# Performance work log

Measured on AMD Instinct MI355X. Metric: run time of the kernel, lower is better.

## Reference

```python
import jax, jax.numpy as jnp
import numpy as np

B = 65536
LAYERS = [256, 512, 512, 256]


def setup_inputs() -> dict:
    key = jax.random.key(0)
    ks = jax.random.split(key, 10)
    inp = {"data": jax.random.normal(ks[0], (B, LAYERS[0]), dtype=jnp.float32)}
    for i in range(3):
        n_in, n_out = LAYERS[i], LAYERS[i + 1]
        # link weights ~ U[0,1) like random.random(); bias params[0] zeroed in torch code
        inp[f"W{i+1}"] = jax.random.uniform(ks[1 + 3 * i], (n_in, n_out), dtype=jnp.float32)
        inp[f"b{i+1}"] = jnp.zeros((n_out,), dtype=jnp.float32)
        # per-node activation params a = params[1:6], torch.rand init
        inp[f"a{i+1}"] = jax.random.uniform(ks[2 + 3 * i], (n_out, 5), dtype=jnp.float32)
    return inp


def _act(x, a):
    # x: [B, n], a: [n, 5]; a0*tanh(x)*sin(a1*x+a2) + a3*x + a4  (per-node params broadcast over batch)
    return a[:, 0] * jnp.tanh(x) * jnp.sin(a[:, 1] * x + a[:, 2]) + a[:, 3] * x + a[:, 4]


def reference(data, W1, b1, a1, W2, b2, a2, W3, b3, a3):
    h = _act(data @ W1 + b1, a1)
    h = _act(h @ W2 + b2, a2)
    h = _act(h @ W3 + b3, a3)
    return jax.nn.softmax(h, axis=1)
```

## Files before the change

### kernel.cpp

```cpp
#include <hip/hip_runtime.h>

#define BATCH 65536

typedef float f32x4 __attribute__((ext_vector_type(4)));
typedef _Float16 f16x8 __attribute__((ext_vector_type(8)));

__device__ __forceinline__ void async_ld16(const void* g, void* l) {
  __builtin_amdgcn_global_load_lds(
      (const __attribute__((address_space(1))) void*)g,
      (__attribute__((address_space(3))) void*)l, 16, 0, 0);
}

__device__ __forceinline__ float act_f(float x, float a0, float a1, float a2,
                                       float a3, float a4) {
  float ax = fabsf(x);
  float e = __builtin_amdgcn_exp2f(ax * -2.8853900817779268f);
  float th = (1.0f - e) * __builtin_amdgcn_rcpf(1.0f + e);
  th = copysignf(th, x);
  float arg = fmaf(a1, x, a2);
  float rev = arg * 0.15915494309189535f;
  rev -= floorf(rev);
  float s = __builtin_amdgcn_sinf(rev);
  return fmaf(a3, x, fmaf(a0 * th, s, a4));
}

__global__ __launch_bounds__(256) void splitT_k(const float* __restrict__ W,
                                                _Float16* __restrict__ hi,
                                                _Float16* __restrict__ lo,
                                                int K, int N) {
  const int i = blockIdx.x * 256 + threadIdx.x;
  if (i >= K * N) return;
  const int k = i / N, n = i % N;
  const float w = W[i];
  const _Float16 h = (_Float16)w;
  hi[(size_t)n * K + k] = h;
  lo[(size_t)n * K + k] = (_Float16)(w - (float)h);
}

template <bool AF32, bool FINAL>
__global__ __launch_bounds__(256, 2) void gemm_act(
    const float* __restrict__ Af, const _Float16* __restrict__ Ahi,
    const _Float16* __restrict__ Alo, const _Float16* __restrict__ Bhi,
    const _Float16* __restrict__ Blo, const float* __restrict__ bias,
    const float* __restrict__ ap, _Float16* __restrict__ Chi,
    _Float16* __restrict__ Clo, float* __restrict__ Cout, int K, int N) {
  __shared__ __align__(16) _Float16 sA[AF32 ? 2 : 2 * 128 * 32];
  __shared__ __align__(16) _Float16 sB[2 * 128 * 32];

  const int tid = threadIdx.x;
  const int wv = tid >> 6;
  const int lane = tid & 63;
  const int wm = wv >> 1, wn = wv & 1;
  const int m16 = lane & 15, quad = lane >> 4;
  const int col0 = blockIdx.x * 128;
  const int row0 = blockIdx.y * 128;
  const int crow = lane >> 2;
  const int cseg = lane & 3;

  f32x4 acc[4][4];
  const f32x4 zero = {0.f, 0.f, 0.f, 0.f};
#pragma unroll
  for (int i = 0; i < 4; ++i)
#pragma unroll
    for (int j = 0; j < 4; ++j) acc[i][j] = zero;

  const int nk = K >> 5;
  for (int kt = 0; kt < nk; ++kt) {
    const int k0 = kt << 5;
    if (!AF32) {
#pragma unroll
      for (int t = 0; t < 2; ++t) {
        const int c = wv * 2 + t;
        const int r = c * 16 + crow;
        const size_t ga = (size_t)(row0 + r) * K + k0 + cseg * 8;
        async_ld16(Ahi + ga, (void*)&sA[c * 512]);
        async_ld16(Alo + ga, (void*)&sA[128 * 32 + c * 512]);
      }
    }
#pragma unroll
    for (int t = 0; t < 2; ++t) {
      const int c = wv * 2 + t;
      const int r = c * 16 + crow;
      const size_t gb = (size_t)(col0 + r) * K + k0 + cseg * 8;
      async_ld16(Bhi + gb, (void*)&sB[c * 512]);
      async_ld16(Blo + gb, (void*)&sB[128 * 32 + c * 512]);
    }

    f16x8 ah[4], al[4], bh[4], bl[4];
    if (AF32) {
#pragma unroll
      for (int tm = 0; tm < 4; ++tm) {
        const float* p =
            Af + (size_t)(row0 + wm * 64 + tm * 16 + m16) * K + k0 + quad * 8;
        const f32x4 x0 = *(const f32x4*)p;
        const f32x4 x1 = *(const f32x4*)(p + 4);
#pragma unroll
        for (int j = 0; j < 4; ++j) {
          const _Float16 h0 = (_Float16)x0[j];
          ah[tm][j] = h0;
          al[tm][j] = (_Float16)(x0[j] - (float)h0);
          const _Float16 h1 = (_Float16)x1[j];
          ah[tm][4 + j] = h1;
          al[tm][4 + j] = (_Float16)(x1[j] - (float)h1);
        }
      }
    }
    __syncthreads();

    if (!AF32) {
#pragma unroll
      for (int tm = 0; tm < 4; ++tm) {
        const int idx = (wm * 64 + tm * 16 + m16) * 32 + quad * 8;
        ah[tm] = *(const f16x8*)&sA[idx];
        al[tm] = *(const f16x8*)&sA[128 * 32 + idx];
      }
    }
#pragma unroll
    for (int tn = 0; tn < 4; ++tn) {
      const int idx = (wn * 64 + tn * 16 + m16) * 32 + quad * 8;
      bh[tn] = *(const f16x8*)&sB[idx];
      bl[tn] = *(const f16x8*)&sB[128 * 32 + idx];
    }
#pragma unroll
    for (int tm = 0; tm < 4; ++tm)
#pragma unroll
      for (int tn = 0; tn < 4; ++tn) {
        acc[tm][tn] = __builtin_amdgcn_mfma_f32_16x16x32_f16(ah[tm], bh[tn],
                                                             acc[tm][tn], 0, 0, 0);
        acc[tm][tn] = __builtin_amdgcn_mfma_f32_16x16x32_f16(ah[tm], bl[tn],
                                                             acc[tm][tn], 0, 0, 0);
        acc[tm][tn] = __builtin_amdgcn_mfma_f32_16x16x32_f16(al[tm], bh[tn],
                                                             acc[tm][tn], 0, 0, 0);
      }
    __syncthreads();
  }

#pragma unroll
  for (int tn = 0; tn < 4; ++tn) {
    const int col = col0 + wn * 64 + tn * 16 + m16;
    const float bs = bias[col];
    const float p0 = ap[col * 5 + 0];
    const float p1 = ap[col * 5 + 1];
    const float p2 = ap[col * 5 + 2];
    const float p3 = ap[col * 5 + 3];
    const float p4 = ap[col * 5 + 4];
#pragma unroll
    for (int tm = 0; tm < 4; ++tm) {
      const int row = row0 + wm * 64 + tm * 16 + quad * 4;
#pragma unroll
      for (int r = 0; r < 4; ++r) {
        const float y = act_f(acc[tm][tn][r] + bs, p0, p1, p2, p3, p4);
        const size_t o = (size_t)(row + r) * N + col;
        if (FINAL) {
          Cout[o] = y;
        } else {
          const _Float16 h = (_Float16)y;
          Chi[o] = h;
          Clo[o] = (_Float16)(y - (float)h);
        }
      }
    }
  }
}

__global__ __launch_bounds__(256) void softmax_rows(float* __restrict__ io) {
  const int wv = threadIdx.x >> 6, lane = threadIdx.x & 63;
  const size_t row = (size_t)blockIdx.x * 4 + wv;
  f32x4* p = (f32x4*)(io + row * 256);
  f32x4 v = p[lane];
  float m = fmaxf(fmaxf(v[0], v[1]), fmaxf(v[2], v[3]));
#pragma unroll
  for (int off = 32; off > 0; off >>= 1) m = fmaxf(m, __shfl_xor(m, off));
  f32x4 e;
  float s = 0.f;
#pragma unroll
  for (int j = 0; j < 4; ++j) {
    e[j] = __builtin_amdgcn_exp2f((v[j] - m) * 1.4426950408889634f);
    s += e[j];
  }
#pragma unroll
  for (int off = 32; off > 0; off >>= 1) s += __shfl_xor(s, off);
  const float inv = __builtin_amdgcn_rcpf(s);
#pragma unroll
  for (int j = 0; j < 4; ++j) e[j] *= inv;
  p[lane] = e;
}

extern "C" void kernel_launch(void* const* d_in, const int* in_sizes, int n_in,
                              void* d_out, int out_size, void* d_ws,
                              size_t ws_size, hipStream_t stream) {
  const float* data = (const float*)d_in[0];
  const float* W1 = (const float*)d_in[1];
  const float* b1 = (const float*)d_in[2];
  const float* a1 = (const float*)d_in[3];
  const float* W2 = (const float*)d_in[4];
  const float* b2 = (const float*)d_in[5];
  const float* a2 = (const float*)d_in[6];
  const float* W3 = (const float*)d_in[7];
  const float* b3 = (const float*)d_in[8];
  const float* a3 = (const float*)d_in[9];
  float* out = (float*)d_out;

  char* ws = (char*)d_ws;
  const size_t KB = 1024, MB = 1024 * 1024;
  _Float16* w1hi = (_Float16*)(ws + 0 * KB);
  _Float16* w1lo = (_Float16*)(ws + 256 * KB);
  _Float16* w2hi = (_Float16*)(ws + 512 * KB);
  _Float16* w2lo = (_Float16*)(ws + 1024 * KB);
  _Float16* w3hi = (_Float16*)(ws + 1536 * KB);
  _Float16* w3lo = (_Float16*)(ws + 1792 * KB);
  char* hb = ws + 2 * MB;

  const size_t avail = (ws_size > 2 * MB) ? ws_size - 2 * MB : 0;
  int R = BATCH;
  while ((size_t)R * 4096 > avail && R > 1024) R >>= 1;
  _Float16* h1hi = (_Float16*)(hb);
  _Float16* h1lo = (_Float16*)(hb + (size_t)R * 1024);
  _Float16* h2hi = (_Float16*)(hb + (size_t)R * 2048);
  _Float16* h2lo = (_Float16*)(hb + (size_t)R * 3072);

  splitT_k<<<(256 * 512 + 255) / 256, 256, 0, stream>>>(W1, w1hi, w1lo, 256, 512);
  splitT_k<<<(512 * 512 + 255) / 256, 256, 0, stream>>>(W2, w2hi, w2lo, 512, 512);
  splitT_k<<<(512 * 256 + 255) / 256, 256, 0, stream>>>(W3, w3hi, w3lo, 512, 256);

  for (int c0 = 0; c0 < BATCH; c0 += R) {
    const float* dc = data + (size_t)c0 * 256;
    float* oc = out + (size_t)c0 * 256;
    gemm_act<true, false><<<dim3(512 / 128, R / 128), 256, 0, stream>>>(
        dc, nullptr, nullptr, w1hi, w1lo, b1, a1, h1hi, h1lo, nullptr, 256, 512);
    gemm_act<false, false><<<dim3(512 / 128, R / 128), 256, 0, stream>>>(
        nullptr, h1hi, h1lo, w2hi, w2lo, b2, a2, h2hi, h2lo, nullptr, 512, 512);
    gemm_act<false, true><<<dim3(256 / 128, R / 128), 256, 0, stream>>>(
        nullptr, h2hi, h2lo, w3hi, w3lo, b3, a3, nullptr, nullptr, oc, 512, 256);
  }

  softmax_rows<<<BATCH / 4, 256, 0, stream>>>(out);
}
```

Measured before the change: 515.1 us.

## Fuse all three MLP layers and softmax into one kernel with LDS-resident activations

Replaces the three per-layer GEMM launches and the separate softmax kernel with a single kernel. Each block handles 32 batch rows and keeps the intermediate activations (split into hi/lo fp16) in a 64KB XOR-swizzled shared buffer, then applies softmax before writing out. This removes the global-memory round trips of the intermediate h1/h2 tensors and the logits. In exchange, weights are streamed directly from global/L2 into registers per block without LDS staging, so every block rereads the full weight matrices. The small row tile also reduces per-block reuse of those weights.

```diff
diff --git a/kernel.cpp b/kernel.cpp
--- a/kernel.cpp
+++ b/kernel.cpp
@@ -4,12 +4,6 @@
 
 typedef float f32x4 __attribute__((ext_vector_type(4)));
 typedef _Float16 f16x8 __attribute__((ext_vector_type(8)));
-
-__device__ __forceinline__ void async_ld16(const void* g, void* l) {
-  __builtin_amdgcn_global_load_lds(
-      (const __attribute__((address_space(1))) void*)g,
-      (__attribute__((address_space(3))) void*)l, 16, 0, 0);
-}
 
 __device__ __forceinline__ float act_f(float x, float a0, float a1, float a2,
                                        float a3, float a4) {
@@ -37,107 +31,53 @@
   lo[(size_t)n * K + k] = (_Float16)(w - (float)h);
 }
 
-template <bool AF32, bool FINAL>
-__global__ __launch_bounds__(256, 2) void gemm_act(
-    const float* __restrict__ Af, const _Float16* __restrict__ Ahi,
-    const _Float16* __restrict__ Alo, const _Float16* __restrict__ Bhi,
-    const _Float16* __restrict__ Blo, const float* __restrict__ bias,
-    const float* __restrict__ ap, _Float16* __restrict__ Chi,
-    _Float16* __restrict__ Clo, float* __restrict__ Cout, int K, int N) {
-  __shared__ __align__(16) _Float16 sA[AF32 ? 2 : 2 * 128 * 32];
-  __shared__ __align__(16) _Float16 sB[2 * 128 * 32];
-
-  const int tid = threadIdx.x;
-  const int wv = tid >> 6;
-  const int lane = tid & 63;
-  const int wm = wv >> 1, wn = wv & 1;
-  const int m16 = lane & 15, quad = lane >> 4;
-  const int col0 = blockIdx.x * 128;
-  const int row0 = blockIdx.y * 128;
-  const int crow = lane >> 2;
-  const int cseg = lane & 3;
-
-  f32x4 acc[4][4];
-  const f32x4 zero = {0.f, 0.f, 0.f, 0.f};
-#pragma unroll
-  for (int i = 0; i < 4; ++i)
-#pragma unroll
-    for (int j = 0; j < 4; ++j) acc[i][j] = zero;
-
-  const int nk = K >> 5;
-  for (int kt = 0; kt < nk; ++kt) {
-    const int k0 = kt << 5;
-    if (!AF32) {
-#pragma unroll
-      for (int t = 0; t < 2; ++t) {
-        const int c = wv * 2 + t;
-        const int r = c * 16 + crow;
-        const size_t ga = (size_t)(row0 + r) * K + k0 + cseg * 8;
-        async_ld16(Ahi + ga, (void*)&sA[c * 512]);
-        async_ld16(Alo + ga, (void*)&sA[128 * 32 + c * 512]);
-      }
-    }
-#pragma unroll
-    for (int t = 0; t < 2; ++t) {
-      const int c = wv * 2 + t;
-      const int r = c * 16 + crow;
-      const size_t gb = (size_t)(col0 + r) * K + k0 + cseg * 8;
-      async_ld16(Bhi + gb, (void*)&sB[c * 512]);
-      async_ld16(Blo + gb, (void*)&sB[128 * 32 + c * 512]);
-    }
-
-    f16x8 ah[4], al[4], bh[4], bl[4];
-    if (AF32) {
-#pragma unroll
-      for (int tm = 0; tm < 4; ++tm) {
-        const float* p =
-            Af + (size_t)(row0 + wm * 64 + tm * 16 + m16) * K + k0 + quad * 8;
-        const f32x4 x0 = *(const f32x4*)p;
-        const f32x4 x1 = *(const f32x4*)(p + 4);
-#pragma unroll
-        for (int j = 0; j < 4; ++j) {
-          const _Float16 h0 = (_Float16)x0[j];
-          ah[tm][j] = h0;
-          al[tm][j] = (_Float16)(x0[j] - (float)h0);
-          const _Float16 h1 = (_Float16)x1[j];
-          ah[tm][4 + j] = h1;
-          al[tm][4 + j] = (_Float16)(x1[j] - (float)h1);
-        }
-      }
-    }
-    __syncthreads();
-
-    if (!AF32) {
-#pragma unroll
-      for (int tm = 0; tm < 4; ++tm) {
-        const int idx = (wm * 64 + tm * 16 + m16) * 32 + quad * 8;
-        ah[tm] = *(const f16x8*)&sA[idx];
-        al[tm] = *(const f16x8*)&sA[128 * 32 + idx];
-      }
-    }
-#pragma unroll
-    for (int tn = 0; tn < 4; ++tn) {
-      const int idx = (wn * 64 + tn * 16 + m16) * 32 + quad * 8;
-      bh[tn] = *(const f16x8*)&sB[idx];
-      bl[tn] = *(const f16x8*)&sB[128 * 32 + idx];
-    }
-#pragma unroll
-    for (int tm = 0; tm < 4; ++tm)
-#pragma unroll
-      for (int tn = 0; tn < 4; ++tn) {
-        acc[tm][tn] = __builtin_amdgcn_mfma_f32_16x16x32_f16(ah[tm], bh[tn],
-                                                             acc[tm][tn], 0, 0, 0);
-        acc[tm][tn] = __builtin_amdgcn_mfma_f32_16x16x32_f16(ah[tm], bl[tn],
-                                                             acc[tm][tn], 0, 0, 0);
-        acc[tm][tn] = __builtin_amdgcn_mfma_f32_16x16x32_f16(al[tm], bh[tn],
-                                                             acc[tm][tn], 0, 0, 0);
-      }
-    __syncthreads();
-  }
-
-#pragma unroll
-  for (int tn = 0; tn < 4; ++tn) {
-    const int col = col0 + wn * 64 + tn * 16 + m16;
+__device__ __forceinline__ f32x4 mfma3(f16x8 ah, f16x8 al, f16x8 bh, f16x8 bl,
+                                       f32x4 c) {
+  c = __builtin_amdgcn_mfma_f32_16x16x32_f16(ah, bh, c, 0, 0, 0);
+  c = __builtin_amdgcn_mfma_f32_16x16x32_f16(ah, bl, c, 0, 0, 0);
+  c = __builtin_amdgcn_mfma_f32_16x16x32_f16(al, bh, c, 0, 0, 0);
+  return c;
+}
+
+template <int NT, int NK>
+__device__ __forceinline__ void layer_h(const _Float16* __restrict__ hb,
+                                        const _Float16* __restrict__ Bhi,
+                                        const _Float16* __restrict__ Blo,
+                                        int K, int wv, int m16, int quad,
+                                        f32x4 acc[2][8]) {
+#pragma unroll 2
+  for (int it = 0; it < NK; ++it) {
+    f16x8 bh[NT], bl[NT];
+    const int nbase = (wv * NT * 16 + m16) * K + it * 32 + quad * 8;
+#pragma unroll
+    for (int tn = 0; tn < NT; ++tn) {
+      bh[tn] = *(const f16x8*)(Bhi + nbase + tn * 16 * K);
+      bl[tn] = *(const f16x8*)(Blo + nbase + tn * 16 * K);
+    }
+    f16x8 ah[2], al[2];
+    const int ks = (it * 32 + quad * 8) ^ (m16 << 3);
+#pragma unroll
+    for (int tm = 0; tm < 2; ++tm) {
+      const int ro = (tm * 16 + m16) * 1024;
+      ah[tm] = *(const f16x8*)&hb[ro + ks];
+      al[tm] = *(const f16x8*)&hb[ro + 512 + ks];
+    }
+#pragma unroll
+    for (int tn = 0; tn < NT; ++tn)
+#pragma unroll
+      for (int tm = 0; tm < 2; ++tm)
+        acc[tm][tn] = mfma3(ah[tm], al[tm], bh[tn], bl[tn], acc[tm][tn]);
+  }
+}
+
+template <int NT, bool TO_H>
+__device__ __forceinline__ void epilogue(f32x4 acc[2][8],
+                                         const float* __restrict__ bias,
+                                         const float* __restrict__ ap, int wv,
+                                         int m16, int quad, _Float16* hb) {
+#pragma unroll
+  for (int tn = 0; tn < NT; ++tn) {
+    const int col = wv * NT * 16 + tn * 16 + m16;
     const float bs = bias[col];
     const float p0 = ap[col * 5 + 0];
     const float p1 = ap[col * 5 + 1];
@@ -145,45 +85,136 @@
     const float p3 = ap[col * 5 + 3];
     const float p4 = ap[col * 5 + 4];
 #pragma unroll
-    for (int tm = 0; tm < 4; ++tm) {
-      const int row = row0 + wm * 64 + tm * 16 + quad * 4;
+    for (int tm = 0; tm < 2; ++tm)
 #pragma unroll
       for (int r = 0; r < 4; ++r) {
+        const int row = tm * 16 + quad * 4 + r;
         const float y = act_f(acc[tm][tn][r] + bs, p0, p1, p2, p3, p4);
-        const size_t o = (size_t)(row + r) * N + col;
-        if (FINAL) {
-          Cout[o] = y;
+        if (TO_H) {
+          const int cs = col ^ ((row & 15) << 3);
+          const _Float16 h = (_Float16)y;
+          hb[row * 1024 + cs] = h;
+          hb[row * 1024 + 512 + cs] = (_Float16)(y - (float)h);
         } else {
-          const _Float16 h = (_Float16)y;
-          Chi[o] = h;
-          Clo[o] = (_Float16)(y - (float)h);
+          ((float*)hb)[row * 256 + col] = y;
         }
       }
-    }
-  }
-}
-
-__global__ __launch_bounds__(256) void softmax_rows(float* __restrict__ io) {
-  const int wv = threadIdx.x >> 6, lane = threadIdx.x & 63;
-  const size_t row = (size_t)blockIdx.x * 4 + wv;
-  f32x4* p = (f32x4*)(io + row * 256);
-  f32x4 v = p[lane];
-  float m = fmaxf(fmaxf(v[0], v[1]), fmaxf(v[2], v[3]));
-#pragma unroll
-  for (int off = 32; off > 0; off >>= 1) m = fmaxf(m, __shfl_xor(m, off));
-  f32x4 e;
-  float s = 0.f;
-#pragma unroll
-  for (int j = 0; j < 4; ++j) {
-    e[j] = __builtin_amdgcn_exp2f((v[j] - m) * 1.4426950408889634f);
-    s += e[j];
-  }
-#pragma unroll
-  for (int off = 32; off > 0; off >>= 1) s += __shfl_xor(s, off);
-  const float inv = __builtin_amdgcn_rcpf(s);
-#pragma unroll
-  for (int j = 0; j < 4; ++j) e[j] *= inv;
-  p[lane] = e;
+  }
+}
+
+__global__ __launch_bounds__(256, 2) void fused_net(
+    const float* __restrict__ data, const _Float16* __restrict__ w1hi,
+    const _Float16* __restrict__ w1lo, const float* __restrict__ b1,
+    const float* __restrict__ a1p, const _Float16* __restrict__ w2hi,
+    const _Float16* __restrict__ w2lo, const float* __restrict__ b2,
+    const float* __restrict__ a2p, const _Float16* __restrict__ w3hi,
+    const _Float16* __restrict__ w3lo, const float* __restrict__ b3,
+    const float* __restrict__ a3p, float* __restrict__ out) {
+  __shared__ __align__(16) _Float16 hb[32 * 1024];
+
+  const int tid = threadIdx.x;
+  const int wv = tid >> 6, lane = tid & 63;
+  const int m16 = lane & 15, quad = lane >> 4;
+  const int row0 = blockIdx.x * 32;
+
+  float* dptr = (float*)hb;
+
+  {
+    const float* dg = data + (size_t)row0 * 256;
+#pragma unroll
+    for (int i = 0; i < 8; ++i) {
+      const int idx = tid + i * 256;
+      const int r = idx >> 6, c4 = (idx & 63) << 2;
+      const f32x4 v = *(const f32x4*)(dg + r * 256 + c4);
+      const int cs = c4 ^ ((r & 15) << 3);
+      *(f32x4*)&dptr[r * 256 + cs] = v;
+    }
+  }
+  __syncthreads();
+
+  f32x4 acc[2][8];
+  const f32x4 zero = {0.f, 0.f, 0.f, 0.f};
+
+#pragma unroll
+  for (int i = 0; i < 2; ++i)
+#pragma unroll
+    for (int j = 0; j < 8; ++j) acc[i][j] = zero;
+#pragma unroll 2
+  for (int it = 0; it < 8; ++it) {
+    f16x8 bh[8], bl[8];
+    const int nbase = (wv * 128 + m16) * 256 + it * 32 + quad * 8;
+#pragma unroll
+    for (int tn = 0; tn < 8; ++tn) {
+      bh[tn] = *(const f16x8*)(w1hi + nbase + tn * 16 * 256);
+      bl[tn] = *(const f16x8*)(w1lo + nbase + tn * 16 * 256);
+    }
+    f16x8 ah[2], al[2];
+    const int ks = (it * 32 + quad * 8) ^ (m16 << 3);
+#pragma unroll
+    for (int tm = 0; tm < 2; ++tm) {
+      const int ro = (tm * 16 + m16) * 256;
+      const f32x4 x0 = *(const f32x4*)&dptr[ro + ks];
+      const f32x4 x1 = *(const f32x4*)&dptr[ro + ks + 4];
+#pragma unroll
+      for (int j = 0; j < 4; ++j) {
+        const _Float16 h0 = (_Float16)x0[j];
+        ah[tm][j] = h0;
+        al[tm][j] = (_Float16)(x0[j] - (float)h0);
+        const _Float16 h1 = (_Float16)x1[j];
+        ah[tm][4 + j] = h1;
+        al[tm][4 + j] = (_Float16)(x1[j] - (float)h1);
+      }
+    }
+#pragma unroll
+    for (int tn = 0; tn < 8; ++tn)
+#pragma unroll
+      for (int tm = 0; tm < 2; ++tm)
+        acc[tm][tn] = mfma3(ah[tm], al[tm], bh[tn], bl[tn], acc[tm][tn]);
+  }
+  __syncthreads();
+  epilogue<8, true>(acc, b1, a1p, wv, m16, quad, hb);
+  __syncthreads();
+
+#pragma unroll
+  for (int i = 0; i < 2; ++i)
+#pragma unroll
+    for (int j = 0; j < 8; ++j) acc[i][j] = zero;
+  layer_h<8, 16>(hb, w2hi, w2lo, 512, wv, m16, quad, acc);
+  __syncthreads();
+  epilogue<8, true>(acc, b2, a2p, wv, m16, quad, hb);
+  __syncthreads();
+
+#pragma unroll
+  for (int i = 0; i < 2; ++i)
+#pragma unroll
+    for (int j = 0; j < 8; ++j) acc[i][j] = zero;
+  layer_h<4, 16>(hb, w3hi, w3lo, 512, wv, m16, quad, acc);
+  __syncthreads();
+  epilogue<4, false>(acc, b3, a3p, wv, m16, quad, hb);
+  __syncthreads();
+
+  const float* lg = (const float*)hb;
+#pragma unroll
+  for (int r8 = 0; r8 < 8; ++r8) {
+    const int row = wv * 8 + r8;
+    f32x4 v = *(const f32x4*)&lg[row * 256 + lane * 4];
+    float m = fmaxf(fmaxf(v[0], v[1]), fmaxf(v[2], v[3]));
+#pragma unroll
+    for (int off = 32; off > 0; off >>= 1) m = fmaxf(m, __shfl_xor(m, off));
+    f32x4 e;
+    float s = 0.f;
+#pragma unroll
+    for (int j = 0; j < 4; ++j) {
+      e[j] = __builtin_amdgcn_exp2f((v[j] - m) * 1.4426950408889634f);
+      s += e[j];
+    }
+#pragma unroll
+    for (int off = 32; off > 0; off >>= 1) s += __shfl_xor(s, off);
+    const float inv = __builtin_amdgcn_rcpf(s);
+#pragma unroll
+    for (int j = 0; j < 4; ++j) e[j] *= inv;
+    *(f32x4*)(out + (size_t)(row0 + row) * 256 + lane * 4) = e;
+  }
 }
 
 extern "C" void kernel_launch(void* const* d_in, const int* in_sizes, int n_in,
@@ -202,37 +233,19 @@
   float* out = (float*)d_out;
 
   char* ws = (char*)d_ws;
-  const size_t KB = 1024, MB = 1024 * 1024;
+  const size_t KB = 1024;
   _Float16* w1hi = (_Float16*)(ws + 0 * KB);
   _Float16* w1lo = (_Float16*)(ws + 256 * KB);
   _Float16* w2hi = (_Float16*)(ws + 512 * KB);
   _Float16* w2lo = (_Float16*)(ws + 1024 * KB);
   _Float16* w3hi = (_Float16*)(ws + 1536 * KB);
   _Float16* w3lo = (_Float16*)(ws + 1792 * KB);
-  char* hb = ws + 2 * MB;
-
-  const size_t avail = (ws_size > 2 * MB) ? ws_size - 2 * MB : 0;
-  int R = BATCH;
-  while ((size_t)R * 4096 > avail && R > 1024) R >>= 1;
-  _Float16* h1hi = (_Float16*)(hb);
-  _Float16* h1lo = (_Float16*)(hb + (size_t)R * 1024);
-  _Float16* h2hi = (_Float16*)(hb + (size_t)R * 2048);
-  _Float16* h2lo = (_Float16*)(hb + (size_t)R * 3072);
 
   splitT_k<<<(256 * 512 + 255) / 256, 256, 0, stream>>>(W1, w1hi, w1lo, 256, 512);
   splitT_k<<<(512 * 512 + 255) / 256, 256, 0, stream>>>(W2, w2hi, w2lo, 512, 512);
   splitT_k<<<(512 * 256 + 255) / 256, 256, 0, stream>>>(W3, w3hi, w3lo, 512, 256);
 
-  for (int c0 = 0; c0 < BATCH; c0 += R) {
-    const float* dc = data + (size_t)c0 * 256;
-    float* oc = out + (size_t)c0 * 256;
-    gemm_act<true, false><<<dim3(512 / 128, R / 128), 256, 0, stream>>>(
-        dc, nullptr, nullptr, w1hi, w1lo, b1, a1, h1hi, h1lo, nullptr, 256, 512);
-    gemm_act<false, false><<<dim3(512 / 128, R / 128), 256, 0, stream>>>(
-        nullptr, h1hi, h1lo, w2hi, w2lo, b2, a2, h2hi, h2lo, nullptr, 512, 512);
-    gemm_act<false, true><<<dim3(256 / 128, R / 128), 256, 0, stream>>>(
-        nullptr, h2hi, h2lo, w3hi, w3lo, b3, a3, nullptr, nullptr, oc, 512, 256);
-  }
-
-  softmax_rows<<<BATCH / 4, 256, 0, stream>>>(out);
-}
+  fused_net<<<BATCH / 32, 256, 0, stream>>>(data, w1hi, w1lo, b1, a1, w2hi,
+                                            w2lo, b2, a2, w3hi, w3lo, b3, a3,
+                                            out);
+}
```

Result: slower. 605.2 us (+17.5%).

## Retile fused GEMM+activation to 64x256 blocks and stage fp32 input through LDS

Applied to the files above, without the earlier changes.

Changes the block tile from 128x128 to 64 rows by 256 columns, so each block covers all or half of the output columns. B fragments are reused across two M sub-tiles, and the launch bound asks for 4 blocks per CU instead of 2. The first layer now copies fp32 input into LDS with async loads instead of reading it directly from global per wave. The batch chunking loop is dropped and the layer-2 hi buffer is placed in the output buffer, which assumes a large enough workspace. This adds LDS use and register pressure, with fewer blocks along N.

```diff
diff --git a/kernel.cpp b/kernel.cpp
--- a/kernel.cpp
+++ b/kernel.cpp
@@ -37,63 +37,75 @@
   lo[(size_t)n * K + k] = (_Float16)(w - (float)h);
 }
 
+__device__ __forceinline__ f32x4 mfma3(f16x8 ah, f16x8 al, f16x8 bh, f16x8 bl,
+                                       f32x4 c) {
+  c = __builtin_amdgcn_mfma_f32_16x16x32_f16(ah, bh, c, 0, 0, 0);
+  c = __builtin_amdgcn_mfma_f32_16x16x32_f16(ah, bl, c, 0, 0, 0);
+  c = __builtin_amdgcn_mfma_f32_16x16x32_f16(al, bh, c, 0, 0, 0);
+  return c;
+}
+
 template <bool AF32, bool FINAL>
-__global__ __launch_bounds__(256, 2) void gemm_act(
+__global__ __launch_bounds__(256, 4) void gemm_act(
     const float* __restrict__ Af, const _Float16* __restrict__ Ahi,
     const _Float16* __restrict__ Alo, const _Float16* __restrict__ Bhi,
     const _Float16* __restrict__ Blo, const float* __restrict__ bias,
     const float* __restrict__ ap, _Float16* __restrict__ Chi,
     _Float16* __restrict__ Clo, float* __restrict__ Cout, int K, int N) {
-  __shared__ __align__(16) _Float16 sA[AF32 ? 2 : 2 * 128 * 32];
-  __shared__ __align__(16) _Float16 sB[2 * 128 * 32];
+  __shared__ __align__(16) _Float16 sA[4096];
+  __shared__ __align__(16) _Float16 sB[16384];
 
   const int tid = threadIdx.x;
   const int wv = tid >> 6;
   const int lane = tid & 63;
   const int wm = wv >> 1, wn = wv & 1;
   const int m16 = lane & 15, quad = lane >> 4;
-  const int col0 = blockIdx.x * 128;
-  const int row0 = blockIdx.y * 128;
-  const int crow = lane >> 2;
-  const int cseg = lane & 3;
-
-  f32x4 acc[4][4];
+  const int col0 = blockIdx.x * 256;
+  const int row0 = blockIdx.y * 64;
+
+  f32x4 acc[2][8];
   const f32x4 zero = {0.f, 0.f, 0.f, 0.f};
 #pragma unroll
-  for (int i = 0; i < 4; ++i)
-#pragma unroll
-    for (int j = 0; j < 4; ++j) acc[i][j] = zero;
+  for (int i = 0; i < 2; ++i)
+#pragma unroll
+    for (int j = 0; j < 8; ++j) acc[i][j] = zero;
 
   const int nk = K >> 5;
   for (int kt = 0; kt < nk; ++kt) {
     const int k0 = kt << 5;
-    if (!AF32) {
+    if (AF32) {
+      float* sAf = (float*)sA;
 #pragma unroll
       for (int t = 0; t < 2; ++t) {
         const int c = wv * 2 + t;
-        const int r = c * 16 + crow;
-        const size_t ga = (size_t)(row0 + r) * K + k0 + cseg * 8;
-        async_ld16(Ahi + ga, (void*)&sA[c * 512]);
-        async_ld16(Alo + ga, (void*)&sA[128 * 32 + c * 512]);
+        const int r = c * 8 + (lane >> 3);
+        const size_t ga = (size_t)(row0 + r) * K + k0 + (lane & 7) * 4;
+        async_ld16(Af + ga, (void*)&sAf[c * 256]);
       }
-    }
-#pragma unroll
-    for (int t = 0; t < 2; ++t) {
-      const int c = wv * 2 + t;
-      const int r = c * 16 + crow;
-      const size_t gb = (size_t)(col0 + r) * K + k0 + cseg * 8;
+    } else {
+      const int r = wv * 16 + (lane >> 2);
+      const size_t ga = (size_t)(row0 + r) * K + k0 + (lane & 3) * 8;
+      async_ld16(Ahi + ga, (void*)&sA[wv * 512]);
+      async_ld16(Alo + ga, (void*)&sA[2048 + wv * 512]);
+    }
+#pragma unroll
+    for (int t = 0; t < 4; ++t) {
+      const int c = wv * 4 + t;
+      const int col = c * 16 + (lane >> 2);
+      const size_t gb = (size_t)(col0 + col) * K + k0 + (lane & 3) * 8;
       async_ld16(Bhi + gb, (void*)&sB[c * 512]);
-      async_ld16(Blo + gb, (void*)&sB[128 * 32 + c * 512]);
-    }
-
-    f16x8 ah[4], al[4], bh[4], bl[4];
-    if (AF32) {
-#pragma unroll
-      for (int tm = 0; tm < 4; ++tm) {
-        const float* p =
-            Af + (size_t)(row0 + wm * 64 + tm * 16 + m16) * K + k0 + quad * 8;
-        const f32x4 x0 = *(const f32x4*)p;
-        const f32x4 x1 = *(const f32x4*)(p + 4);
+      async_ld16(Blo + gb, (void*)&sB[8192 + c * 512]);
+    }
+    __syncthreads();
+
+    f16x8 ah[2], al[2];
+#pragma unroll
+    for (int tm = 0; tm < 2; ++tm) {
+      const int arow = wm * 32 + tm * 16 + m16;
+      if (AF32) {
+        const float* pa = (const float*)sA + arow * 32 + quad * 8;
+        const f32x4 x0 = *(const f32x4*)pa;
+        const f32x4 x1 = *(const f32x4*)(pa + 4);
 #pragma unroll
         for (int j = 0; j < 4; ++j) {
           const _Float16 h0 = (_Float16)x0[j];
@@ -103,41 +115,26 @@
           ah[tm][4 + j] = h1;
           al[tm][4 + j] = (_Float16)(x1[j] - (float)h1);
         }
+      } else {
+        ah[tm] = *(const f16x8*)&sA[arow * 32 + quad * 8];
+        al[tm] = *(const f16x8*)&sA[2048 + arow * 32 + quad * 8];
       }
     }
-    __syncthreads();
-
-    if (!AF32) {
-#pragma unroll
-      for (int tm = 0; tm < 4; ++tm) {
-        const int idx = (wm * 64 + tm * 16 + m16) * 32 + quad * 8;
-        ah[tm] = *(const f16x8*)&sA[idx];
-        al[tm] = *(const f16x8*)&sA[128 * 32 + idx];
-      }
-    }
-#pragma unroll
-    for (int tn = 0; tn < 4; ++tn) {
-      const int idx = (wn * 64 + tn * 16 + m16) * 32 + quad * 8;
-      bh[tn] = *(const f16x8*)&sB[idx];
-      bl[tn] = *(const f16x8*)&sB[128 * 32 + idx];
-    }
-#pragma unroll
-    for (int tm = 0; tm < 4; ++tm)
-#pragma unroll
-      for (int tn = 0; tn < 4; ++tn) {
-        acc[tm][tn] = __builtin_amdgcn_mfma_f32_16x16x32_f16(ah[tm], bh[tn],
-                                                             acc[tm][tn], 0, 0, 0);
-        acc[tm][tn] = __builtin_amdgcn_mfma_f32_16x16x32_f16(ah[tm], bl[tn],
-                                                             acc[tm][tn], 0, 0, 0);
-        acc[tm][tn] = __builtin_amdgcn_mfma_f32_16x16x32_f16(al[tm], bh[tn],
-                                                             acc[tm][tn], 0, 0, 0);
-      }
+#pragma unroll
+    for (int tn = 0; tn < 8; ++tn) {
+      const int bcol = wn * 128 + tn * 16 + m16;
+      const f16x8 bh = *(const f16x8*)&sB[bcol * 32 + quad * 8];
+      const f16x8 bl = *(const f16x8*)&sB[8192 + bcol * 32 + quad * 8];
+#pragma unroll
+      for (int tm = 0; tm < 2; ++tm)
+        acc[tm][tn] = mfma3(ah[tm], al[tm], bh, bl, acc[tm][tn]);
+    }
     __syncthreads();
   }
 
 #pragma unroll
-  for (int tn = 0; tn < 4; ++tn) {
-    const int col = col0 + wn * 64 + tn * 16 + m16;
+  for (int tn = 0; tn < 8; ++tn) {
+    const int col = col0 + wn * 128 + tn * 16 + m16;
     const float bs = bias[col];
     const float p0 = ap[col * 5 + 0];
     const float p1 = ap[col * 5 + 1];
@@ -145,15 +142,15 @@
     const float p3 = ap[col * 5 + 3];
     const float p4 = ap[col * 5 + 4];
 #pragma unroll
-    for (int tm = 0; tm < 4; ++tm) {
-      const int row = row0 + wm * 64 + tm * 16 + quad * 4;
+    for (int tm = 0; tm < 2; ++tm) {
+      const int row = row0 + wm * 32 + tm * 16 + quad * 4;
 #pragma unroll
       for (int r = 0; r < 4; ++r) {
         const float y = act_f(acc[tm][tn][r] + bs, p0, p1, p2, p3, p4);
-        const size_t o = (size_t)(row + r) * N + col;
         if (FINAL) {
-          Cout[o] = y;
+          Cout[(size_t)(row + r) * 256 + col] = y;
         } else {
+          const size_t o = (size_t)(row + r) * N + col;
           const _Float16 h = (_Float16)y;
           Chi[o] = h;
           Clo[o] = (_Float16)(y - (float)h);
@@ -209,30 +206,21 @@
   _Float16* w2lo = (_Float16*)(ws + 1024 * KB);
   _Float16* w3hi = (_Float16*)(ws + 1536 * KB);
   _Float16* w3lo = (_Float16*)(ws + 1792 * KB);
-  char* hb = ws + 2 * MB;
-
-  const size_t avail = (ws_size > 2 * MB) ? ws_size - 2 * MB : 0;
-  int R = BATCH;
-  while ((size_t)R * 4096 > avail && R > 1024) R >>= 1;
-  _Float16* h1hi = (_Float16*)(hb);
-  _Float16* h1lo = (_Float16*)(hb + (size_t)R * 1024);
-  _Float16* h2hi = (_Float16*)(hb + (size_t)R * 2048);
-  _Float16* h2lo = (_Float16*)(hb + (size_t)R * 3072);
+  _Float16* h1hi = (_Float16*)(ws + 2 * MB);
+  _Float16* h1lo = (_Float16*)(ws + 2 * MB + (size_t)BATCH * 512 * 2);
+  _Float16* h2lo = (_Float16*)(ws + 2 * MB + (size_t)BATCH * 512 * 4);
+  _Float16* h2hi = (_Float16*)d_out;
 
   splitT_k<<<(256 * 512 + 255) / 256, 256, 0, stream>>>(W1, w1hi, w1lo, 256, 512);
   splitT_k<<<(512 * 512 + 255) / 256, 256, 0, stream>>>(W2, w2hi, w2lo, 512, 512);
   splitT_k<<<(512 * 256 + 255) / 256, 256, 0, stream>>>(W3, w3hi, w3lo, 512, 256);
 
-  for (int c0 = 0; c0 < BATCH; c0 += R) {
-    const float* dc = data + (size_t)c0 * 256;
-    float* oc = out + (size_t)c0 * 256;
-    gemm_act<true, false><<<dim3(512 / 128, R / 128), 256, 0, stream>>>(
-        dc, nullptr, nullptr, w1hi, w1lo, b1, a1, h1hi, h1lo, nullptr, 256, 512);
-    gemm_act<false, false><<<dim3(512 / 128, R / 128), 256, 0, stream>>>(
-        nullptr, h1hi, h1lo, w2hi, w2lo, b2, a2, h2hi, h2lo, nullptr, 512, 512);
-    gemm_act<false, true><<<dim3(256 / 128, R / 128), 256, 0, stream>>>(
-        nullptr, h2hi, h2lo, w3hi, w3lo, b3, a3, nullptr, nullptr, oc, 512, 256);
-  }
+  gemm_act<true, false><<<dim3(2, BATCH / 64), 256, 0, stream>>>(
+      data, nullptr, nullptr, w1hi, w1lo, b1, a1, h1hi, h1lo, nullptr, 256, 512);
+  gemm_act<false, false><<<dim3(2, BATCH / 64), 256, 0, stream>>>(
+      nullptr, h1hi, h1lo, w2hi, w2lo, b2, a2, h2hi, h2lo, nullptr, 512, 512);
+  gemm_act<false, true><<<dim3(1, BATCH / 64), 256, 0, stream>>>(
+      nullptr, h2hi, h2lo, w3hi, w3lo, b3, a3, nullptr, nullptr, out, 512, 256);
 
   softmax_rows<<<BATCH / 4, 256, 0, stream>>>(out);
 }
```

After: 438.9 us. 1.17x faster.
